# Kernel optimization log

Measured on AMD Instinct MI355X. Metric: run time of the kernel, lower is better.

The kernel has to match this reference:

```python
import jax, jax.numpy as jnp
import numpy as np

B, T, A_DIM, Z_DIM, K = 128, 80, 32, 64, 16


def setup_inputs() -> dict:
    key = jax.random.key(0)
    k1, k2, k3, k4 = jax.random.split(key, 4)
    obs = jax.random.normal(k1, (B, T, A_DIM), jnp.float32)
    alpha_logits = jax.random.normal(k2, (B, T, K), jnp.float32)
    # torch init: A = eye(z) repeated K times; small noise keeps 80-step recursion stable
    A_K = jnp.eye(Z_DIM, dtype=jnp.float32)[None] + 0.005 * jax.random.normal(k3, (K, Z_DIM, Z_DIM), jnp.float32)
    # torch init: C = 0.05 * randn
    C_K = 0.05 * jax.random.normal(k4, (K, A_DIM, Z_DIM), jnp.float32)
    return {"obs": obs, "alpha_logits": alpha_logits, "A_K": A_K, "C_K": C_K}


def _kalman(obs, A, C):
    # obs [B,T,a], A [B,T,z,z], C [B,T,a,z]
    Bq, Tq, a_dim = obs.shape
    z_dim = A.shape[-1]
    dt = obs.dtype
    Q = 0.08 * jnp.eye(z_dim, dtype=dt)
    R = 0.03 * jnp.eye(a_dim, dtype=dt)
    I = jnp.eye(z_dim, dtype=dt)

    obs_t = jnp.swapaxes(obs, 0, 1)          # [T,B,a]
    A_t = jnp.swapaxes(A, 0, 1)              # [T,B,z,z]
    C_t = jnp.swapaxes(C, 0, 1)              # [T,B,a,z]
    A_next = jnp.concatenate([A_t[1:], A_t[-1:]], axis=0)  # A[t+1]; last unused

    mu0 = jnp.zeros((Bq, z_dim), dt)
    sig0 = jnp.broadcast_to(20.0 * I, (Bq, z_dim, z_dim))

    def filt_step(carry, inp):
        mu_p, sig_p, mu_prev = carry
        At, Anx, Ct, y = inp
        CtT = jnp.swapaxes(Ct, -1, -2)
        S = Ct @ sig_p @ CtT + R                       # [B,a,a]
        Kg = sig_p @ CtT @ jnp.linalg.inv(S)            # [B,z,a]
        Amu = jnp.einsum('bij,bj->bi', At, mu_prev)     # A_t mu_{t-1}
        err = y - jnp.einsum('bij,bj->bi', Ct, Amu)
        mu_f = Amu + jnp.einsum('bij,bj->bi', Kg, err)
        sig_f = (I - Kg @ Ct) @ sig_p
        mu_pn = jnp.einsum('bij,bj->bi', Anx, mu_f)     # prediction with A_{t+1}
        sig_pn = Anx @ sig_f @ jnp.swapaxes(Anx, -1, -2) + Q
        return (mu_pn, sig_pn, mu_f), (mu_f, sig_f, mu_p, sig_p)

    _, (mu_f, sig_f, mu_p, sig_p) = jax.lax.scan(
        filt_step, (mu0, sig0, mu0), (A_t, A_next, C_t, obs_t))

    def smooth_step(carry, inp):
        mu_s, sig_s = carry
        mf, sf, Anx, mpn, spn = inp
        J = sf @ jnp.swapaxes(Anx, -1, -2) @ jnp.linalg.inv(spn)
        mu = mf + jnp.einsum('bij,bj->bi', J, mu_s - mpn)
        sig = sf + J @ (sig_s - spn) @ jnp.swapaxes(J, -1, -2)
        return (mu, sig), (mu, sig)

    init = (mu_f[-1], sig_f[-1])
    _, (mu_sm, sig_sm) = jax.lax.scan(
        smooth_step, init,
        (mu_f[:-1], sig_f[:-1], A_t[1:], mu_p[1:], sig_p[1:]),
        reverse=True)
    mu_sm = jnp.concatenate([mu_sm, mu_f[-1:]], axis=0)
    sig_sm = jnp.concatenate([sig_sm, sig_f[-1:]], axis=0)
    return jnp.swapaxes(mu_sm, 0, 1), jnp.swapaxes(sig_sm, 0, 1)  # [B,T,z], [B,T,z,z]


def reference(obs, alpha_logits, A_K, C_K):
    w = jax.nn.softmax(alpha_logits, axis=-1)                # [B,T,K]
    A = jnp.einsum('btk,kij->btij', w, A_K)                  # [B,T,z,z]
    C = jnp.einsum('btk,kij->btij', w, C_K)                  # [B,T,a,z]
    return _kalman(obs, A, C)
```

## Files before the change

### kernel.cpp

```cpp
#include <hip/hip_runtime.h>

#define B_ 128
#define T_ 80
#define AD 32
#define ZD 64
#define KD 16
#define S8 68
#define SC 36

__device__ __forceinline__ float4 ld4(const float* p) { return *(const float4*)p; }
__device__ __forceinline__ void st4f(float* p, float4 v) { *(float4*)p = v; }
__device__ __forceinline__ float4 sub4(float4 a, float4 b) {
    return make_float4(a.x - b.x, a.y - b.y, a.z - b.z, a.w - b.w);
}
__device__ __forceinline__ float4 comb4(float4 c, float4 x0, float4 x1, float4 x2, float4 x3) {
    return make_float4(c.x*x0.x + c.y*x1.x + c.z*x2.x + c.w*x3.x,
                       c.x*x0.y + c.y*x1.y + c.z*x2.y + c.w*x3.y,
                       c.x*x0.z + c.y*x1.z + c.z*x2.z + c.w*x3.z,
                       c.x*x0.w + c.y*x1.w + c.z*x2.w + c.w*x3.w);
}

__device__ __forceinline__ void pinv4(float4 q0, float4 q1, float4 q2, float4 q3,
                                      float4& pi0, float4& pi1, float4& pi2, float4& pi3)
{
    const float ra = 1.0f / (q0.x*q1.y - q0.y*q1.x);
    const float ai00 =  q1.y*ra, ai01 = -q0.y*ra, ai10 = -q1.x*ra, ai11 = q0.x*ra;
    const float ca00 = q2.x*ai00 + q2.y*ai10, ca01 = q2.x*ai01 + q2.y*ai11;
    const float ca10 = q3.x*ai00 + q3.y*ai10, ca11 = q3.x*ai01 + q3.y*ai11;
    const float s00 = q2.z - (ca00*q0.z + ca01*q1.z), s01 = q2.w - (ca00*q0.w + ca01*q1.w);
    const float s10 = q3.z - (ca10*q0.z + ca11*q1.z), s11 = q3.w - (ca10*q0.w + ca11*q1.w);
    const float rs = 1.0f / (s00*s11 - s01*s10);
    const float si00 = s11*rs, si01 = -s01*rs, si10 = -s10*rs, si11 = s00*rs;
    const float ab00 = ai00*q0.z + ai01*q1.z, ab01 = ai00*q0.w + ai01*q1.w;
    const float ab10 = ai10*q0.z + ai11*q1.z, ab11 = ai10*q0.w + ai11*q1.w;
    const float t00 = ab00*si00 + ab01*si10, t01 = ab00*si01 + ab01*si11;
    const float t10 = ab10*si00 + ab11*si10, t11 = ab10*si01 + ab11*si11;
    const float tl00 = ai00 + (t00*ca00 + t01*ca10), tl01 = ai01 + (t00*ca01 + t01*ca11);
    const float tl10 = ai10 + (t10*ca00 + t11*ca10), tl11 = ai11 + (t10*ca01 + t11*ca11);
    const float bl00 = -(si00*ca00 + si01*ca10), bl01 = -(si00*ca01 + si01*ca11);
    const float bl10 = -(si10*ca00 + si11*ca10), bl11 = -(si10*ca01 + si11*ca11);
    pi0 = make_float4(tl00, tl01, -t00, -t01);
    pi1 = make_float4(tl10, tl11, -t10, -t11);
    pi2 = make_float4(bl00, bl01, si00, si01);
    pi3 = make_float4(bl10, bl11, si10, si11);
}

template<int KL, int AS, int BS, bool ATRANS>
__device__ __forceinline__ void mm64(const float* __restrict__ Pa, const float* __restrict__ Qb,
                                     float acc[2][4], int r2, int c4)
{
#pragma unroll 8
    for (int k = 0; k < KL; k++) {
        float aA, aB;
        if (ATRANS) { aA = Pa[k * AS + r2];   aB = Pa[k * AS + r2 + 1]; }
        else        { aA = Pa[r2 * AS + k];   aB = Pa[(r2 + 1) * AS + k]; }
        const float4 bv = ld4(&Qb[k * BS + c4]);
        acc[0][0] += aA * bv.x; acc[0][1] += aA * bv.y; acc[0][2] += aA * bv.z; acc[0][3] += aA * bv.w;
        acc[1][0] += aB * bv.x; acc[1][1] += aB * bv.y; acc[1][2] += aB * bv.z; acc[1][3] += aB * bv.w;
    }
}

__global__ __launch_bounds__(512, 2)
void kvae_kernel(const float* __restrict__ obs, const float* __restrict__ logits,
                 const float* __restrict__ AK, const float* __restrict__ CK,
                 float* __restrict__ out)
{
    __shared__ __align__(16) float W[T_ * KD];
    __shared__ __align__(16) float Am[ZD * S8];
    __shared__ __align__(16) float At[ZD * S8];
    __shared__ __align__(16) float SP[ZD * S8];
    __shared__ __align__(16) float SF[ZD * S8];
    __shared__ __align__(16) float Mm[ZD * S8];
    __shared__ __align__(16) float Pool[9984];
    __shared__ __align__(16) float pvL[512];
    __shared__ __align__(16) float pvR[512];
    __shared__ __align__(16) float fbb[512];
    __shared__ __align__(16) float pvE[8];
    __shared__ __align__(16) float errv[32];
    __shared__ __align__(16) float uev[32];
    __shared__ __align__(16) float mup[64];
    __shared__ __align__(16) float muf[64];
    __shared__ __align__(16) float mus[64];
    __shared__ __align__(16) float mpn[64];
    __shared__ __align__(16) float dv[64];

    float* T1 = Pool;
    float* CM = Pool + 2176;
    float* CT = Pool + 4352;
    float* U_ = Pool + 6656;
    float* S_ = Pool + 8832;
    float* Xb = Pool;
    float* SG = Pool + 4352;

    const int tid = threadIdx.x;
    const int b   = blockIdx.x;

    const int r16 = tid >> 4;
    const int cg  = tid & 15;
    const int c4  = cg << 2;
    const int c2  = cg << 1;
    const int r2  = r16 << 1;
    const int gi  = tid >> 3;
    const int gs  = tid & 7;

    const float* obs_b = obs    + (size_t)b * T_ * AD;
    const float* lg_b  = logits + (size_t)b * T_ * KD;
    float* omu = out + (size_t)b * T_ * ZD;
    float* osg = out + (size_t)B_ * T_ * ZD + (size_t)b * T_ * ZD * ZD;
    const float4* AK4 = (const float4*)AK;
    const float4* CK4 = (const float4*)CK;

    auto mixA = [&](int tt) {
#pragma unroll
        for (int rr = 0; rr < 2; rr++) {
            const int r = r2 + rr;
            float4 a = make_float4(0.f, 0.f, 0.f, 0.f);
#pragma unroll
            for (int k = 0; k < KD; k++) {
                const float wk = W[tt * KD + k];
                const float4 v = AK4[k * 1024 + r * 16 + cg];
                a.x += wk * v.x; a.y += wk * v.y; a.z += wk * v.z; a.w += wk * v.w;
            }
            st4f(&Am[r * S8 + c4], a);
            At[(c4 + 0) * S8 + r] = a.x; At[(c4 + 1) * S8 + r] = a.y;
            At[(c4 + 2) * S8 + r] = a.z; At[(c4 + 3) * S8 + r] = a.w;
        }
    };
    auto mixC = [&](int tt) {
        float4 a = make_float4(0.f, 0.f, 0.f, 0.f);
#pragma unroll
        for (int k = 0; k < KD; k++) {
            const float wk = W[tt * KD + k];
            const float4 v = CK4[k * 512 + r16 * 16 + cg];
            a.x += wk * v.x; a.y += wk * v.y; a.z += wk * v.z; a.w += wk * v.w;
        }
        st4f(&CM[r16 * S8 + c4], a);
        CT[(c4 + 0) * SC + r16] = a.x; CT[(c4 + 1) * SC + r16] = a.y;
        CT[(c4 + 2) * SC + r16] = a.z; CT[(c4 + 3) * SC + r16] = a.w;
    };

    if (tid < T_) {
        float l[KD]; float mx = -1e30f;
#pragma unroll
        for (int k = 0; k < KD; k++) { l[k] = lg_b[tid * KD + k]; mx = fmaxf(mx, l[k]); }
        float s = 0.f;
#pragma unroll
        for (int k = 0; k < KD; k++) { l[k] = expf(l[k] - mx); s += l[k]; }
        const float inv = 1.0f / s;
#pragma unroll
        for (int k = 0; k < KD; k++) W[tid * KD + k] = l[k] * inv;
    }
#pragma unroll
    for (int rr = 0; rr < 2; rr++) {
        const int r = r2 + rr;
#pragma unroll
        for (int j = 0; j < 4; j++) SP[r * S8 + c4 + j] = (r == c4 + j) ? 20.0f : 0.0f;
    }
    if (tid < ZD) mup[tid] = 0.0f;
    __syncthreads();

    for (int t = 0; t < T_; t++) {
        if (t < T_ - 1) mixA(t + 1);
        mixC(t);
        float yreg = 0.f;
        if (tid < AD) yreg = obs_b[t * AD + tid];
        __syncthreads();

        {
            float a0 = 0, a1 = 0, a2 = 0, a3 = 0;
            const float* pa = CM + r16 * S8;
#pragma unroll 8
            for (int k = 0; k < ZD; k++) {
                const float a = pa[k];
                const float4 bv = ld4(&SP[k * S8 + c4]);
                a0 += a * bv.x; a1 += a * bv.y; a2 += a * bv.z; a3 += a * bv.w;
            }
            T1[r16 * S8 + c4 + 0] = a0; T1[r16 * S8 + c4 + 1] = a1;
            T1[r16 * S8 + c4 + 2] = a2; T1[r16 * S8 + c4 + 3] = a3;
        }
        __syncthreads();

        {
            float a0 = 0, a1 = 0;
            const float* pa = T1 + r16 * S8;
#pragma unroll 8
            for (int k = 0; k < ZD; k++) {
                const float a = pa[k];
                const float2 bv = *(const float2*)&CT[k * SC + c2];
                a0 += a * bv.x; a1 += a * bv.y;
            }
            if (r16 == c2)     a0 += 0.03f;
            if (r16 == c2 + 1) a1 += 0.03f;
            S_[r16 * SC + c2] = a0; S_[r16 * SC + c2 + 1] = a1;
        }
        if (tid < AD) {
            float s = 0.f;
#pragma unroll
            for (int k4 = 0; k4 < ZD; k4 += 4) {
                const float4 cm = ld4(&CM[tid * S8 + k4]);
                const float4 mu = ld4(&mup[k4]);
                s += cm.x*mu.x + cm.y*mu.y + cm.z*mu.z + cm.w*mu.w;
            }
            errv[tid] = yreg - s;
        }
        __syncthreads();

        {
            const int hi = r16, hs = cg;
            float4 aL = make_float4(0, 0, 0, 0);
            float4 aR = ld4(&T1[hi * S8 + hs * 4]);
            float e = 0.f;
            if (hs < 8) aL = ld4(&S_[hi * SC + hs * 4]);
            if (hs == 15) e = errv[hi];
            if (hi < 4) {
                if (hs < 8) st4f(&pvL[hi * 32 + hs * 4], aL);
                st4f(&pvR[hi * 64 + hs * 4], aR);
                if (hs == 15) pvE[hi] = e;
            }
            if (hs == 0) st4f(&fbb[hi * 4], aL);
            __syncthreads();

#pragma unroll 2
            for (int j = 0; j < 8; ++j) {
                const int par = j & 1, nb = par ^ 1;
                const bool isp = (hi >> 2) == j;
                const int i4 = hi & 3;
                const float4 q0 = ld4(&fbb[par * 128 + (4 * j + 0) * 4]);
                const float4 q1 = ld4(&fbb[par * 128 + (4 * j + 1) * 4]);
                const float4 q2 = ld4(&fbb[par * 128 + (4 * j + 2) * 4]);
                const float4 q3 = ld4(&fbb[par * 128 + (4 * j + 3) * 4]);
                float4 pi0, pi1, pi2, pi3;
                pinv4(q0, q1, q2, q3, pi0, pi1, pi2, pi3);
                float4 coef;
                if (isp) coef = (i4 == 0 ? pi0 : i4 == 1 ? pi1 : i4 == 2 ? pi2 : pi3);
                else {
                    const float4 f = ld4(&fbb[par * 128 + hi * 4]);
                    coef = comb4(f, pi0, pi1, pi2, pi3);
                }
                {
                    const float4 c = comb4(coef,
                        ld4(&pvR[par * 256 + 0 * 64 + hs * 4]),
                        ld4(&pvR[par * 256 + 1 * 64 + hs * 4]),
                        ld4(&pvR[par * 256 + 2 * 64 + hs * 4]),
                        ld4(&pvR[par * 256 + 3 * 64 + hs * 4]));
                    if (isp) aR = c; else aR = sub4(aR, c);
                }
                if (hs < 8) {
                    const float4 c = comb4(coef,
                        ld4(&pvL[par * 128 + 0 * 32 + hs * 4]),
                        ld4(&pvL[par * 128 + 1 * 32 + hs * 4]),
                        ld4(&pvL[par * 128 + 2 * 32 + hs * 4]),
                        ld4(&pvL[par * 128 + 3 * 32 + hs * 4]));
                    if (isp) aL = c; else aL = sub4(aL, c);
                }
                if (hs == 15) {
                    const float4 ev = ld4(&pvE[par * 4]);
                    const float ce = coef.x*ev.x + coef.y*ev.y + coef.z*ev.z + coef.w*ev.w;
                    if (isp) e = ce; else e -= ce;
                }
                if (j < 7) {
                    if ((hi >> 2) == j + 1) {
                        if (hs < 8) st4f(&pvL[nb * 128 + i4 * 32 + hs * 4], aL);
                        st4f(&pvR[nb * 256 + i4 * 64 + hs * 4], aR);
                        if (hs == 15) pvE[nb * 4 + i4] = e;
                    }
                    if (hs == j + 1) st4f(&fbb[nb * 128 + hi * 4], aL);
                }
                __syncthreads();
            }
            st4f(&U_[hi * S8 + hs * 4], aR);
            if (hs == 15) uev[hi] = e;
        }
        __syncthreads();

        {
            float acc[2][4] = {};
            mm64<AD, S8, S8, true>(T1, U_, acc, r2, c4);
            float* og = osg + (size_t)t * ZD * ZD;
#pragma unroll
            for (int rr = 0; rr < 2; rr++) {
                const int r = r2 + rr;
                const float4 sp = ld4(&SP[r * S8 + c4]);
                const float4 v = make_float4(sp.x - acc[rr][0], sp.y - acc[rr][1],
                                             sp.z - acc[rr][2], sp.w - acc[rr][3]);
                st4f(&SF[r * S8 + c4], v);
                *(float4*)(og + r * ZD + c4) = v;
            }
        }
        if (tid < ZD) {
            float s = 0.f;
#pragma unroll
            for (int k = 0; k < AD; k++) s += T1[k * S8 + tid] * uev[k];
            const float v = mup[tid] + s;
            muf[tid] = v;
            omu[t * ZD + tid] = v;
        }
        __syncthreads();

        if (t < T_ - 1) {
            {
                float acc[2][4] = {};
                mm64<ZD, S8, S8, false>(Am, SF, acc, r2, c4);
#pragma unroll
                for (int rr = 0; rr < 2; rr++)
                    st4f(&Mm[(r2 + rr) * S8 + c4],
                         make_float4(acc[rr][0], acc[rr][1], acc[rr][2], acc[rr][3]));
            }
            __syncthreads();
            {
                float acc[2][4] = {};
                mm64<ZD, S8, S8, false>(Mm, At, acc, r2, c4);
#pragma unroll
                for (int rr = 0; rr < 2; rr++) {
                    const int r = r2 + rr;
#pragma unroll
                    for (int j = 0; j < 4; j++)
                        SP[r * S8 + c4 + j] = acc[rr][j] + ((r == c4 + j) ? 0.08f : 0.0f);
                }
            }
            if (tid >= 448) {
                const int i = tid - 448;
                float s = 0.f;
                const float* pa = Am + i * S8;
#pragma unroll 8
                for (int k = 0; k < ZD; k++) s += pa[k] * muf[k];
                mup[i] = s;
            }
            __syncthreads();
        }
    }

#pragma unroll
    for (int rr = 0; rr < 2; rr++)
        st4f(&SG[(r2 + rr) * S8 + c4], ld4(&SF[(r2 + rr) * S8 + c4]));
    if (tid < ZD) mus[tid] = muf[tid];
    float4 pf0, pf1; float pmu = 0.f;
    {
        const float4* og4p = (const float4*)(osg + (size_t)(T_ - 2) * ZD * ZD);
        pf0 = og4p[r2 * 16 + cg];
        pf1 = og4p[(r2 + 1) * 16 + cg];
        if (tid >= 448) pmu = omu[(T_ - 2) * ZD + (tid - 448)];
    }
    __syncthreads();

    for (int t = T_ - 2; t >= 0; t--) {
        mixA(t + 1);
        st4f(&SF[r2 * S8 + c4], pf0);
        st4f(&SF[(r2 + 1) * S8 + c4], pf1);
        if (tid >= 448) muf[tid - 448] = pmu;
        if (t > 0) {
            const float4* og4p = (const float4*)(osg + (size_t)(t - 1) * ZD * ZD);
            pf0 = og4p[r2 * 16 + cg];
            pf1 = og4p[(r2 + 1) * 16 + cg];
            if (tid >= 448) pmu = omu[(t - 1) * ZD + (tid - 448)];
        }
        __syncthreads();

        {
            float acc[2][4] = {};
            mm64<ZD, S8, S8, false>(Am, SF, acc, r2, c4);
#pragma unroll
            for (int rr = 0; rr < 2; rr++)
                st4f(&Mm[(r2 + rr) * S8 + c4],
                     make_float4(acc[rr][0], acc[rr][1], acc[rr][2], acc[rr][3]));
        }
        if (tid >= 448) {
            const int i = tid - 448;
            float s = 0.f;
            const float* pa = Am + i * S8;
#pragma unroll 8
            for (int k = 0; k < ZD; k++) s += pa[k] * muf[k];
            mpn[i] = s;
        }
        __syncthreads();

        {
            float acc[2][4] = {};
            mm64<ZD, S8, S8, false>(Mm, At, acc, r2, c4);
#pragma unroll
            for (int rr = 0; rr < 2; rr++) {
                const int r = r2 + rr;
#pragma unroll
                for (int j = 0; j < 4; j++)
                    SP[r * S8 + c4 + j] = acc[rr][j] + ((r == c4 + j) ? 0.08f : 0.0f);
            }
        }
        if (tid >= 448) { const int i = tid - 448; dv[i] = mus[i] - mpn[i]; }
        __syncthreads();

        {
            float4 aL0 = ld4(&SP[gi * S8 + gs * 8]);
            float4 aL1 = ld4(&SP[gi * S8 + gs * 8 + 4]);
            float4 aR0 = ld4(&Mm[gi * S8 + gs * 8]);
            float4 aR1 = ld4(&Mm[gi * S8 + gs * 8 + 4]);
            if (gi < 4) {
                st4f(&pvL[gi * 64 + gs * 8], aL0); st4f(&pvL[gi * 64 + gs * 8 + 4], aL1);
                st4f(&pvR[gi * 64 + gs * 8], aR0); st4f(&pvR[gi * 64 + gs * 8 + 4], aR1);
            }
            if (gs == 0) st4f(&fbb[gi * 4], aL0);
            __syncthreads();

#pragma unroll 2
            for (int j = 0; j < 16; ++j) {
                const int par = j & 1, nb = par ^ 1;
                const bool isp = (gi >> 2) == j;
                const int i4 = gi & 3;
                const float4 q0 = ld4(&fbb[par * 256 + (4 * j + 0) * 4]);
                const float4 q1 = ld4(&fbb[par * 256 + (4 * j + 1) * 4]);
                const float4 q2 = ld4(&fbb[par * 256 + (4 * j + 2) * 4]);
                const float4 q3 = ld4(&fbb[par * 256 + (4 * j + 3) * 4]);
                float4 pi0, pi1, pi2, pi3;
                pinv4(q0, q1, q2, q3, pi0, pi1, pi2, pi3);
                float4 coef;
                if (isp) coef = (i4 == 0 ? pi0 : i4 == 1 ? pi1 : i4 == 2 ? pi2 : pi3);
                else {
                    const float4 f = ld4(&fbb[par * 256 + gi * 4]);
                    coef = comb4(f, pi0, pi1, pi2, pi3);
                }
                {
                    const float4 x0 = ld4(&pvL[par * 256 + 0 * 64 + gs * 8]);
                    const float4 x1 = ld4(&pvL[par * 256 + 1 * 64 + gs * 8]);
                    const float4 x2 = ld4(&pvL[par * 256 + 2 * 64 + gs * 8]);
                    const float4 x3 = ld4(&pvL[par * 256 + 3 * 64 + gs * 8]);
                    const float4 c = comb4(coef, x0, x1, x2, x3);
                    if (isp) aL0 = c;
                    else { aL0.x -= c.x; aL0.y -= c.y; aL0.z -= c.z; aL0.w -= c.w; }
                }
                {
                    const float4 x0 = ld4(&pvL[par * 256 + 0 * 64 + gs * 8 + 4]);
                    const float4 x1 = ld4(&pvL[par * 256 + 1 * 64 + gs * 8 + 4]);
                    const float4 x2 = ld4(&pvL[par * 256 + 2 * 64 + gs * 8 + 4]);
                    const float4 x3 = ld4(&pvL[par * 256 + 3 * 64 + gs * 8 + 4]);
                    const float4 c = comb4(coef, x0, x1, x2, x3);
                    if (isp) aL1 = c;
                    else { aL1.x -= c.x; aL1.y -= c.y; aL1.z -= c.z; aL1.w -= c.w; }
                }
                {
                    const float4 x0 = ld4(&pvR[par * 256 + 0 * 64 + gs * 8]);
                    const float4 x1 = ld4(&pvR[par * 256 + 1 * 64 + gs * 8]);
                    const float4 x2 = ld4(&pvR[par * 256 + 2 * 64 + gs * 8]);
                    const float4 x3 = ld4(&pvR[par * 256 + 3 * 64 + gs * 8]);
                    const float4 c = comb4(coef, x0, x1, x2, x3);
                    if (isp) aR0 = c;
                    else { aR0.x -= c.x; aR0.y -= c.y; aR0.z -= c.z; aR0.w -= c.w; }
                }
                {
                    const float4 x0 = ld4(&pvR[par * 256 + 0 * 64 + gs * 8 + 4]);
                    const float4 x1 = ld4(&pvR[par * 256 + 1 * 64 + gs * 8 + 4]);
                    const float4 x2 = ld4(&pvR[par * 256 + 2 * 64 + gs * 8 + 4]);
                    const float4 x3 = ld4(&pvR[par * 256 + 3 * 64 + gs * 8 + 4]);
                    const float4 c = comb4(coef, x0, x1, x2, x3);
                    if (isp) aR1 = c;
                    else { aR1.x -= c.x; aR1.y -= c.y; aR1.z -= c.z; aR1.w -= c.w; }
                }
                if (j < 15) {
                    if ((gi >> 2) == j + 1) {
                        const int rn = gi & 3;
                        st4f(&pvL[nb * 256 + rn * 64 + gs * 8], aL0);
                        st4f(&pvL[nb * 256 + rn * 64 + gs * 8 + 4], aL1);
                        st4f(&pvR[nb * 256 + rn * 64 + gs * 8], aR0);
                        st4f(&pvR[nb * 256 + rn * 64 + gs * 8 + 4], aR1);
                    }
                    if (gs == ((j + 1) >> 1))
                        st4f(&fbb[nb * 256 + gi * 4], ((j + 1) & 1) ? aL1 : aL0);
                }
                __syncthreads();
            }
            st4f(&Xb[gi * S8 + gs * 8], aR0);
            st4f(&Xb[gi * S8 + gs * 8 + 4], aR1);
        }
        __syncthreads();

        {
            float acc[2][4] = {};
            mm64<ZD, S8, S8, false>(SG, Xb, acc, r2, c4);
#pragma unroll
            for (int rr = 0; rr < 2; rr++) {
                const int r = r2 + rr;
                const float4 m = ld4(&Mm[r * S8 + c4]);
                SP[r * S8 + c4 + 0] = acc[rr][0] - m.x;
                SP[r * S8 + c4 + 1] = acc[rr][1] - m.y;
                SP[r * S8 + c4 + 2] = acc[rr][2] - m.z;
                SP[r * S8 + c4 + 3] = acc[rr][3] - m.w;
            }
        }
        __syncthreads();

        {
            float acc[2][4] = {};
            mm64<ZD, S8, S8, true>(Xb, SP, acc, r2, c4);
            float* og = osg + (size_t)t * ZD * ZD;
#pragma unroll
            for (int rr = 0; rr < 2; rr++) {
                const int r = r2 + rr;
                const float4 sf = ld4(&SF[r * S8 + c4]);
                const float4 v = make_float4(sf.x + acc[rr][0], sf.y + acc[rr][1],
                                             sf.z + acc[rr][2], sf.w + acc[rr][3]);
                st4f(&SG[r * S8 + c4], v);
                *(float4*)(og + r * ZD + c4) = v;
            }
        }
        if (tid < ZD) {
            float s = 0.f;
#pragma unroll 8
            for (int k = 0; k < ZD; k++) s += Xb[k * S8 + tid] * dv[k];
            const float v = muf[tid] + s;
            mus[tid] = v;
            omu[t * ZD + tid] = v;
        }
        __syncthreads();
    }
}

extern "C" void kernel_launch(void* const* d_in, const int* in_sizes, int n_in,
                              void* d_out, int out_size, void* d_ws, size_t ws_size,
                              hipStream_t stream) {
    const float* obs = (const float*)d_in[0];
    const float* lg  = (const float*)d_in[1];
    const float* AK  = (const float*)d_in[2];
    const float* CK  = (const float*)d_in[3];
    (void)d_ws; (void)ws_size; (void)in_sizes; (void)n_in; (void)out_size;
    kvae_kernel<<<dim3(B_), dim3(512), 0, stream>>>(obs, lg, AK, CK, (float*)d_out);
}
```

Before: 3.672 ms.

## Use 4x4 register tiles on half the block and overlap matvecs on idle waves

The 64x64 shared-memory matmuls now use a 4x4 per-thread register tile computed by only the first 256 threads, instead of a 2x4 tile over all 512 threads. The mean matrix-vector updates move to threads 448-511 so they can run alongside the matmuls. The smoother no longer prefetches the previous filtered covariance into registers and instead loads it directly each step. The aim is more data reuse per shared-memory load and concurrent vector work, at the cost of half the threads idling during matmuls, higher register pressure, and a global-load stall in the backward pass.

```diff
diff --git a/kernel.cpp b/kernel.cpp
--- a/kernel.cpp
+++ b/kernel.cpp
@@ -60,6 +60,28 @@
     }
 }
 
+template<int KL, int AS, int BS, bool ATRANS>
+__device__ __forceinline__ void mm44(const float* __restrict__ Pa, const float* __restrict__ Qb,
+                                     float acc[4][4], int r4, int c4)
+{
+#pragma unroll 4
+    for (int k = 0; k < KL; k++) {
+        float a0, a1, a2, a3;
+        if (ATRANS) {
+            const float4 av = ld4(&Pa[k * AS + r4]);
+            a0 = av.x; a1 = av.y; a2 = av.z; a3 = av.w;
+        } else {
+            a0 = Pa[(r4 + 0) * AS + k]; a1 = Pa[(r4 + 1) * AS + k];
+            a2 = Pa[(r4 + 2) * AS + k]; a3 = Pa[(r4 + 3) * AS + k];
+        }
+        const float4 bv = ld4(&Qb[k * BS + c4]);
+        acc[0][0] += a0 * bv.x; acc[0][1] += a0 * bv.y; acc[0][2] += a0 * bv.z; acc[0][3] += a0 * bv.w;
+        acc[1][0] += a1 * bv.x; acc[1][1] += a1 * bv.y; acc[1][2] += a1 * bv.z; acc[1][3] += a1 * bv.w;
+        acc[2][0] += a2 * bv.x; acc[2][1] += a2 * bv.y; acc[2][2] += a2 * bv.z; acc[2][3] += a2 * bv.w;
+        acc[3][0] += a3 * bv.x; acc[3][1] += a3 * bv.y; acc[3][2] += a3 * bv.z; acc[3][3] += a3 * bv.w;
+    }
+}
+
 __global__ __launch_bounds__(512, 2)
 void kvae_kernel(const float* __restrict__ obs, const float* __restrict__ logits,
                  const float* __restrict__ AK, const float* __restrict__ CK,
@@ -76,6 +98,7 @@
     __shared__ __align__(16) float pvR[512];
     __shared__ __align__(16) float fbb[512];
     __shared__ __align__(16) float pvE[8];
+    __shared__ __align__(16) float y_s[32];
     __shared__ __align__(16) float errv[32];
     __shared__ __align__(16) float uev[32];
     __shared__ __align__(16) float mup[64];
@@ -102,6 +125,8 @@
     const int r2  = r16 << 1;
     const int gi  = tid >> 3;
     const int gs  = tid & 7;
+    const int r4f = (tid & 255) >> 4 << 2;
+    const int r2h = (tid & 255) >> 4 << 1;
 
     const float* obs_b = obs    + (size_t)b * T_ * AD;
     const float* lg_b  = logits + (size_t)b * T_ * KD;
@@ -162,21 +187,16 @@
     for (int t = 0; t < T_; t++) {
         if (t < T_ - 1) mixA(t + 1);
         mixC(t);
-        float yreg = 0.f;
-        if (tid < AD) yreg = obs_b[t * AD + tid];
-        __syncthreads();
-
-        {
-            float a0 = 0, a1 = 0, a2 = 0, a3 = 0;
-            const float* pa = CM + r16 * S8;
-#pragma unroll 8
-            for (int k = 0; k < ZD; k++) {
-                const float a = pa[k];
-                const float4 bv = ld4(&SP[k * S8 + c4]);
-                a0 += a * bv.x; a1 += a * bv.y; a2 += a * bv.z; a3 += a * bv.w;
-            }
-            T1[r16 * S8 + c4 + 0] = a0; T1[r16 * S8 + c4 + 1] = a1;
-            T1[r16 * S8 + c4 + 2] = a2; T1[r16 * S8 + c4 + 3] = a3;
+        if (tid < AD) y_s[tid] = obs_b[t * AD + tid];
+        __syncthreads();
+
+        if (tid < 256) {
+            float acc[2][4] = {};
+            mm64<ZD, S8, S8, false>(CM, SP, acc, r2h, c4);
+#pragma unroll
+            for (int rr = 0; rr < 2; rr++)
+                st4f(&T1[(r2h + rr) * S8 + c4],
+                     make_float4(acc[rr][0], acc[rr][1], acc[rr][2], acc[rr][3]));
         }
         __syncthreads();
 
@@ -201,7 +221,7 @@
                 const float4 mu = ld4(&mup[k4]);
                 s += cm.x*mu.x + cm.y*mu.y + cm.z*mu.z + cm.w*mu.w;
             }
-            errv[tid] = yreg - s;
+            errv[tid] = y_s[tid] - s;
         }
         __syncthreads();
 
@@ -273,49 +293,50 @@
         }
         __syncthreads();
 
-        {
-            float acc[2][4] = {};
-            mm64<AD, S8, S8, true>(T1, U_, acc, r2, c4);
+        if (tid < 256) {
+            float acc[4][4] = {};
+            mm44<AD, S8, S8, true>(T1, U_, acc, r4f, c4);
             float* og = osg + (size_t)t * ZD * ZD;
 #pragma unroll
-            for (int rr = 0; rr < 2; rr++) {
-                const int r = r2 + rr;
+            for (int q = 0; q < 4; q++) {
+                const int r = r4f + q;
                 const float4 sp = ld4(&SP[r * S8 + c4]);
-                const float4 v = make_float4(sp.x - acc[rr][0], sp.y - acc[rr][1],
-                                             sp.z - acc[rr][2], sp.w - acc[rr][3]);
+                const float4 v = make_float4(sp.x - acc[q][0], sp.y - acc[q][1],
+                                             sp.z - acc[q][2], sp.w - acc[q][3]);
                 st4f(&SF[r * S8 + c4], v);
                 *(float4*)(og + r * ZD + c4) = v;
             }
         }
-        if (tid < ZD) {
+        if (tid >= 448) {
+            const int i = tid - 448;
             float s = 0.f;
 #pragma unroll
-            for (int k = 0; k < AD; k++) s += T1[k * S8 + tid] * uev[k];
-            const float v = mup[tid] + s;
-            muf[tid] = v;
-            omu[t * ZD + tid] = v;
+            for (int k = 0; k < AD; k++) s += T1[k * S8 + i] * uev[k];
+            const float v = mup[i] + s;
+            muf[i] = v;
+            omu[t * ZD + i] = v;
         }
         __syncthreads();
 
         if (t < T_ - 1) {
-            {
-                float acc[2][4] = {};
-                mm64<ZD, S8, S8, false>(Am, SF, acc, r2, c4);
-#pragma unroll
-                for (int rr = 0; rr < 2; rr++)
-                    st4f(&Mm[(r2 + rr) * S8 + c4],
-                         make_float4(acc[rr][0], acc[rr][1], acc[rr][2], acc[rr][3]));
+            if (tid < 256) {
+                float acc[4][4] = {};
+                mm44<ZD, S8, S8, false>(Am, SF, acc, r4f, c4);
+#pragma unroll
+                for (int q = 0; q < 4; q++)
+                    st4f(&Mm[(r4f + q) * S8 + c4],
+                         make_float4(acc[q][0], acc[q][1], acc[q][2], acc[q][3]));
             }
             __syncthreads();
-            {
-                float acc[2][4] = {};
-                mm64<ZD, S8, S8, false>(Mm, At, acc, r2, c4);
-#pragma unroll
-                for (int rr = 0; rr < 2; rr++) {
-                    const int r = r2 + rr;
+            if (tid < 256) {
+                float acc[4][4] = {};
+                mm44<ZD, S8, S8, false>(Mm, At, acc, r4f, c4);
+#pragma unroll
+                for (int q = 0; q < 4; q++) {
+                    const int r = r4f + q;
 #pragma unroll
                     for (int j = 0; j < 4; j++)
-                        SP[r * S8 + c4 + j] = acc[rr][j] + ((r == c4 + j) ? 0.08f : 0.0f);
+                        SP[r * S8 + c4 + j] = acc[q][j] + ((r == c4 + j) ? 0.08f : 0.0f);
                 }
             }
             if (tid >= 448) {
@@ -334,35 +355,26 @@
     for (int rr = 0; rr < 2; rr++)
         st4f(&SG[(r2 + rr) * S8 + c4], ld4(&SF[(r2 + rr) * S8 + c4]));
     if (tid < ZD) mus[tid] = muf[tid];
-    float4 pf0, pf1; float pmu = 0.f;
-    {
-        const float4* og4p = (const float4*)(osg + (size_t)(T_ - 2) * ZD * ZD);
-        pf0 = og4p[r2 * 16 + cg];
-        pf1 = og4p[(r2 + 1) * 16 + cg];
-        if (tid >= 448) pmu = omu[(T_ - 2) * ZD + (tid - 448)];
-    }
     __syncthreads();
 
     for (int t = T_ - 2; t >= 0; t--) {
         mixA(t + 1);
-        st4f(&SF[r2 * S8 + c4], pf0);
-        st4f(&SF[(r2 + 1) * S8 + c4], pf1);
-        if (tid >= 448) muf[tid - 448] = pmu;
-        if (t > 0) {
-            const float4* og4p = (const float4*)(osg + (size_t)(t - 1) * ZD * ZD);
-            pf0 = og4p[r2 * 16 + cg];
-            pf1 = og4p[(r2 + 1) * 16 + cg];
-            if (tid >= 448) pmu = omu[(t - 1) * ZD + (tid - 448)];
-        }
-        __syncthreads();
-
         {
-            float acc[2][4] = {};
-            mm64<ZD, S8, S8, false>(Am, SF, acc, r2, c4);
+            const float4* og4 = (const float4*)(osg + (size_t)t * ZD * ZD);
 #pragma unroll
             for (int rr = 0; rr < 2; rr++)
-                st4f(&Mm[(r2 + rr) * S8 + c4],
-                     make_float4(acc[rr][0], acc[rr][1], acc[rr][2], acc[rr][3]));
+                st4f(&SF[(r2 + rr) * S8 + c4], og4[(r2 + rr) * 16 + cg]);
+        }
+        if (tid >= 448) muf[tid - 448] = omu[t * ZD + (tid - 448)];
+        __syncthreads();
+
+        if (tid < 256) {
+            float acc[4][4] = {};
+            mm44<ZD, S8, S8, false>(Am, SF, acc, r4f, c4);
+#pragma unroll
+            for (int q = 0; q < 4; q++)
+                st4f(&Mm[(r4f + q) * S8 + c4],
+                     make_float4(acc[q][0], acc[q][1], acc[q][2], acc[q][3]));
         }
         if (tid >= 448) {
             const int i = tid - 448;
@@ -374,15 +386,15 @@
         }
         __syncthreads();
 
-        {
-            float acc[2][4] = {};
-            mm64<ZD, S8, S8, false>(Mm, At, acc, r2, c4);
-#pragma unroll
-            for (int rr = 0; rr < 2; rr++) {
-                const int r = r2 + rr;
+        if (tid < 256) {
+            float acc[4][4] = {};
+            mm44<ZD, S8, S8, false>(Mm, At, acc, r4f, c4);
+#pragma unroll
+            for (int q = 0; q < 4; q++) {
+                const int r = r4f + q;
 #pragma unroll
                 for (int j = 0; j < 4; j++)
-                    SP[r * S8 + c4 + j] = acc[rr][j] + ((r == c4 + j) ? 0.08f : 0.0f);
+                    SP[r * S8 + c4 + j] = acc[q][j] + ((r == c4 + j) ? 0.08f : 0.0f);
             }
         }
         if (tid >= 448) { const int i = tid - 448; dv[i] = mus[i] - mpn[i]; }
@@ -471,42 +483,43 @@
         }
         __syncthreads();
 
-        {
-            float acc[2][4] = {};
-            mm64<ZD, S8, S8, false>(SG, Xb, acc, r2, c4);
-#pragma unroll
-            for (int rr = 0; rr < 2; rr++) {
-                const int r = r2 + rr;
+        if (tid < 256) {
+            float acc[4][4] = {};
+            mm44<ZD, S8, S8, false>(SG, Xb, acc, r4f, c4);
+#pragma unroll
+            for (int q = 0; q < 4; q++) {
+                const int r = r4f + q;
                 const float4 m = ld4(&Mm[r * S8 + c4]);
-                SP[r * S8 + c4 + 0] = acc[rr][0] - m.x;
-                SP[r * S8 + c4 + 1] = acc[rr][1] - m.y;
-                SP[r * S8 + c4 + 2] = acc[rr][2] - m.z;
-                SP[r * S8 + c4 + 3] = acc[rr][3] - m.w;
-            }
-        }
-        __syncthreads();
-
-        {
-            float acc[2][4] = {};
-            mm64<ZD, S8, S8, true>(Xb, SP, acc, r2, c4);
+                SP[r * S8 + c4 + 0] = acc[q][0] - m.x;
+                SP[r * S8 + c4 + 1] = acc[q][1] - m.y;
+                SP[r * S8 + c4 + 2] = acc[q][2] - m.z;
+                SP[r * S8 + c4 + 3] = acc[q][3] - m.w;
+            }
+        }
+        __syncthreads();
+
+        if (tid < 256) {
+            float acc[4][4] = {};
+            mm44<ZD, S8, S8, true>(Xb, SP, acc, r4f, c4);
             float* og = osg + (size_t)t * ZD * ZD;
 #pragma unroll
-            for (int rr = 0; rr < 2; rr++) {
-                const int r = r2 + rr;
+            for (int q = 0; q < 4; q++) {
+                const int r = r4f + q;
                 const float4 sf = ld4(&SF[r * S8 + c4]);
-                const float4 v = make_float4(sf.x + acc[rr][0], sf.y + acc[rr][1],
-                                             sf.z + acc[rr][2], sf.w + acc[rr][3]);
+                const float4 v = make_float4(sf.x + acc[q][0], sf.y + acc[q][1],
+                                             sf.z + acc[q][2], sf.w + acc[q][3]);
                 st4f(&SG[r * S8 + c4], v);
                 *(float4*)(og + r * ZD + c4) = v;
             }
         }
-        if (tid < ZD) {
+        if (tid >= 448) {
+            const int i = tid - 448;
             float s = 0.f;
 #pragma unroll 8
-            for (int k = 0; k < ZD; k++) s += Xb[k * S8 + tid] * dv[k];
-            const float v = muf[tid] + s;
-            mus[tid] = v;
-            omu[t * ZD + tid] = v;
+            for (int k = 0; k < ZD; k++) s += Xb[k * S8 + i] * dv[k];
+            const float v = muf[i] + s;
+            mus[i] = v;
+            omu[t * ZD + i] = v;
         }
         __syncthreads();
     }
```

After: 3.810 ms. 3.8% more time.
